# Performance work log

Hardware: AMD Instinct MI355X
Metric: run time of the kernel (lower is better)

Reference implementation:

```python
import jax, jax.numpy as jnp
import numpy as np
from jax import lax

# --- model constants (match init_kwargs) ---
B = 4096
T, N_FEAT = 100, 81
KH = 7                 # cnn_kernel_height
T_MOD = T - KH + 1     # 94
M = 100                # cnn_hidden_size
P = 128                # decoder hidden size
SKIP = 10
SH = 32                # skip_hidden_size
PT = T_MOD // SKIP     # 9


def setup_inputs() -> dict:
    key = jax.random.key(0)
    ks = jax.random.split(key, 18)
    s = 0.05
    def rn(k, shape, scale=s):
        return jax.random.normal(k, shape, dtype=jnp.float32) * scale
    return {
        "enc_data": jax.random.normal(ks[0], (B, T, N_FEAT), dtype=jnp.float32),
        # Conv2d(1 -> M, kernel=(KH, N_FEAT))
        "conv_w": rn(ks[1], (M, 1, KH, N_FEAT)),
        "conv_b": rn(ks[2], (M,)),
        # TemporalAttention: W_d: Linear(2P->M, no bias), U_d: Linear(M->M, no bias), v_d: Linear(M->1, no bias)
        "Wd": rn(ks[3], (M, 2 * P)),
        "Ud": rn(ks[4], (M, M)),
        "vd": rn(ks[5], (1, M)),
        # LSTM(input=M, hidden=P), PyTorch gate order i,f,g,o
        "lstm_wih": rn(ks[6], (4 * P, M)),
        "lstm_whh": rn(ks[7], (4 * P, P)),
        "lstm_bih": rn(ks[8], (4 * P,)),
        "lstm_bhh": rn(ks[9], (4 * P,)),
        # GRU(input=M, hidden=SH), PyTorch gate order r,z,n
        "gru_wih": rn(ks[10], (3 * SH, M)),
        "gru_whh": rn(ks[11], (3 * SH, SH)),
        "gru_bih": rn(ks[12], (3 * SH,)),
        "gru_bhh": rn(ks[13], (3 * SH,)),
        # output head: Linear(M+P+SKIP*SH -> P), ReLU, (Dropout=eval identity), Linear(P -> 1)
        "out1_w": rn(ks[14], (P, M + P + SKIP * SH)),
        "out1_b": rn(ks[15], (P,)),
        "out2_w": rn(ks[16], (1, P)),
        "out2_b": rn(ks[17], (1,)),
    }


def reference(enc_data, conv_w, conv_b, Wd, Ud, vd,
              lstm_wih, lstm_whh, lstm_bih, lstm_bhh,
              gru_wih, gru_whh, gru_bih, gru_bhh,
              out1_w, out1_b, out2_w, out2_b):
    b = enc_data.shape[0]

    # --- CNN encoder: Conv2d valid over full feature width -> [B, T_MOD, M] ---
    x = enc_data[:, None]  # [B,1,T,n]
    h = lax.conv_general_dilated(x, conv_w, window_strides=(1, 1), padding='VALID',
                                 dimension_numbers=('NCHW', 'OIHW', 'NCHW'))  # [B,M,T_MOD,1]
    H = jax.nn.relu(h + conv_b[None, :, None, None])[..., 0].transpose(0, 2, 1)  # [B,T_MOD,M]

    # precompute U_d(H) once (same math; U_d applied to H is step-invariant)
    HU = jnp.einsum('btm,km->btk', H, Ud)  # [B,T_MOD,M]

    def dec_step(carry, _):
        d, s = carry  # each [B,P]
        q = jnp.concatenate([d, s], axis=1)                       # [B,2P]
        e = jnp.tanh((q @ Wd.T)[:, None, :] + HU)                 # [B,T_MOD,M]
        scores = jnp.einsum('btm,m->bt', e, vd[0])                # [B,T_MOD]
        beta = jax.nn.softmax(scores, axis=1)                     # softmax over time
        c = jnp.einsum('bt,btm->bm', beta, H)                     # context [B,M]
        gates = c @ lstm_wih.T + lstm_bih + d @ lstm_whh.T + lstm_bhh
        i_g, f_g, g_g, o_g = jnp.split(gates, 4, axis=1)
        s_new = jax.nn.sigmoid(f_g) * s + jax.nn.sigmoid(i_g) * jnp.tanh(g_g)
        d_new = jax.nn.sigmoid(o_g) * jnp.tanh(s_new)
        return (d_new, s_new), (beta, c)

    d0 = jnp.zeros((b, P), dtype=enc_data.dtype)
    s0 = jnp.zeros((b, P), dtype=enc_data.dtype)
    (d_T, _), (betas, cs) = lax.scan(dec_step, (d0, s0), None, length=T_MOD)
    c_last = cs[-1]                                               # [B,M]
    dec_out = jnp.concatenate([d_T, c_last], axis=1)              # [B, P+M]

    # --- skip GRU over strided conv features ---
    Hs = H[:, -PT * SKIP:, :]                                     # [B, PT*SKIP, M]
    Hs = (Hs.transpose(0, 2, 1)                                   # [B, M, PT*SKIP]
            .reshape(b, M, PT, SKIP)
            .transpose(2, 0, 3, 1)                                # [PT, B, SKIP, M]
            .reshape(PT, b * SKIP, M))

    def gru_step(hprev, xt):
        gi = xt @ gru_wih.T + gru_bih
        gh = hprev @ gru_whh.T + gru_bhh
        ir, iz, inn = jnp.split(gi, 3, axis=1)
        hr, hz, hn = jnp.split(gh, 3, axis=1)
        r = jax.nn.sigmoid(ir + hr)
        z = jax.nn.sigmoid(iz + hz)
        nn_ = jnp.tanh(inn + r * hn)
        hnew = (1.0 - z) * nn_ + z * hprev
        return hnew, None

    h0 = jnp.zeros((b * SKIP, SH), dtype=enc_data.dtype)
    h_skip, _ = lax.scan(gru_step, h0, Hs)                        # [B*SKIP, SH]
    h_skip = h_skip.reshape(b, SKIP * SH)                         # matches torch view

    feat = jnp.concatenate([dec_out, h_skip], axis=1)             # [B, P+M+SKIP*SH]
    out = jax.nn.relu(feat @ out1_w.T + out1_b) @ out2_w.T + out2_b  # [B,1]
    return out[:, 0]
```

## Files before the change

### kernel.cpp

```cpp
#include <hip/hip_runtime.h>

typedef unsigned int u32;
typedef unsigned short u16;
typedef _Float16 half2_t __attribute__((ext_vector_type(2)));

#define TM 94
#define NB 4
#define DEC_NT 512

__device__ __forceinline__ float bf2f(u16 v){ return __builtin_bit_cast(float, ((u32)v)<<16); }
__device__ __forceinline__ float bflo(u32 v){ return __builtin_bit_cast(float, v<<16); }
__device__ __forceinline__ float bfhi(u32 v){ return __builtin_bit_cast(float, v & 0xffff0000u); }
__device__ __forceinline__ u32 f2bf_bits(float f){ u32 u=__builtin_bit_cast(u32,f); return (u + 0x7fffu + ((u>>16)&1u))>>16; }
__device__ __forceinline__ u32 packbf2(float a, float b){ return f2bf_bits(a) | (f2bf_bits(b)<<16); }
__device__ __forceinline__ u32 packh2(float a, float b){ half2_t h; h.x=(_Float16)a; h.y=(_Float16)b; return __builtin_bit_cast(u32,h); }
__device__ __forceinline__ float fdot2(u32 a, u32 b, float c){
  return __builtin_amdgcn_fdot2(__builtin_bit_cast(half2_t,a), __builtin_bit_cast(half2_t,b), c, false);
}
__device__ __forceinline__ float fast_rcp(float x){ return __builtin_amdgcn_rcpf(x); }
__device__ __forceinline__ float sigmoid_f(float x){ return fast_rcp(1.f + __expf(-x)); }
__device__ __forceinline__ float tanh_f(float x){ float e=__expf(2.f*x); return 1.f - 2.f*fast_rcp(e+1.f); }

__global__ __launch_bounds__(128)
void conv_kernel(const float* __restrict__ enc, const float* __restrict__ cw,
                 const float* __restrict__ cb, u16* __restrict__ Hb)
{
  __shared__ float sE[8100];
  const int tid = threadIdx.x;
  const int b = blockIdx.y;
  const int chunk = blockIdx.x;
  const float* ep = enc + (size_t)b*8100;
  for (int i=tid;i<8100;i+=128) sE[i]=ep[i];
  __syncthreads();
  if (tid >= TM) return;
  const int t = tid;
  const int mo = chunk*10;
  const float* wb = cw + mo*567;
  float acc[10];
  #pragma unroll
  for (int k=0;k<10;k++) acc[k]=cb[mo+k];
  const float* e = sE + t*81;
  #pragma unroll 3
  for (int j=0;j<567;j++){
    float ev = e[j];
    #pragma unroll
    for (int k=0;k<10;k++) acc[k] += ev*wb[k*567+j];
  }
  u32* out = (u32*)Hb + ((size_t)b*9400 + t*100 + mo)/2;
  #pragma unroll
  for (int k=0;k<5;k++) out[k] = packbf2(fmaxf(acc[2*k],0.f), fmaxf(acc[2*k+1],0.f));
}

#define OFF_SHU   75200
#define OFF_SQ2   152448
#define OFF_SA    154496
#define OFF_SB    156096
#define OFF_SC2   157632
#define OFF_SG    158464
#define OFF_SVD   162560
#define DEC_LDS   162960

__global__ __launch_bounds__(DEC_NT)
__attribute__((amdgpu_waves_per_eu(2, 2)))
void decoder_kernel(const u16* __restrict__ Hb, const float* __restrict__ Wd,
                    const float* __restrict__ Ud, const float* __restrict__ vd,
                    const float* __restrict__ wih, const float* __restrict__ whh,
                    const float* __restrict__ bih, const float* __restrict__ bhh,
                    float* __restrict__ dT, float* __restrict__ cLast)
{
  extern __shared__ char smem[];
  u16*      sH   = (u16*)smem;
  u16*      sHU  = (u16*)(smem + OFF_SHU);
  _Float16* sq2  = (_Float16*)(smem + OFF_SQ2);
  float*    sa   = (float*)(smem + OFF_SA);
  float*    sbeta= (float*)(smem + OFF_SB);
  u32*      sc2  = (u32*)(smem + OFF_SC2);
  _Float16* sg   = (_Float16*)(smem + OFF_SG);
  float*    svd  = (float*)(smem + OFF_SVD);

  const int tid = threadIdx.x;
  const int b0 = blockIdx.x * NB;

  {
    const uint4* src = (const uint4*)(Hb + (size_t)b0*9400);
    uint4* dst = (uint4*)sH;
    for (int i=tid;i<4700;i+=DEC_NT) dst[i]=src[i];
  }
  if (tid < 100) svd[tid] = vd[tid];
  {
    u32* q2 = (u32*)sq2;
    for (int i=tid;i<NB*128;i+=DEC_NT) q2[i]=0u;
  }
  __syncthreads();

  for (int idx=tid; idx<9400; idx+=DEC_NT){
    int kq = idx/376;
    int r  = idx - kq*376;
    int bi = r/94;
    int t  = r - 94*bi;
    const u32* hrow = (const u32*)sH + bi*4700 + t*50;
    const float* ud0 = Ud + (kq*4+0)*100;
    const float* ud1 = Ud + (kq*4+1)*100;
    const float* ud2 = Ud + (kq*4+2)*100;
    const float* ud3 = Ud + (kq*4+3)*100;
    float c0=0.f,c1=0.f,c2=0.f,c3=0.f;
    #pragma unroll 5
    for (int mq=0; mq<25; mq++){
      uint2 hp = *(const uint2*)(hrow + mq*2);
      float h0=bflo(hp.x), h1=bfhi(hp.x), h2=bflo(hp.y), h3=bfhi(hp.y);
      float4 u0 = *(const float4*)(ud0 + mq*4);
      float4 u1 = *(const float4*)(ud1 + mq*4);
      float4 u2 = *(const float4*)(ud2 + mq*4);
      float4 u3 = *(const float4*)(ud3 + mq*4);
      c0 += h0*u0.x + h1*u0.y + h2*u0.z + h3*u0.w;
      c1 += h0*u1.x + h1*u1.y + h2*u1.z + h3*u1.w;
      c2 += h0*u2.x + h1*u2.y + h2*u2.z + h3*u2.w;
      c3 += h0*u3.x + h1*u3.y + h2*u3.z + h3*u3.w;
    }
    u32* dst = (u32*)sHU + bi*4700 + t*50 + kq*2;
    dst[0] = packbf2(c0,c1);
    dst[1] = packbf2(c2,c3);
  }
  __syncthreads();

  __builtin_amdgcn_sched_barrier(0);
  const int mw = tid>>2, part = tid&3;
  u32 Wih[50]; u32 Whh[64]; u32 Wdf[32];
  float biasg;
  {
    const float2* wr = (const float2*)(wih + (size_t)tid*100);
    #pragma unroll
    for (int i=0;i<50;i++){ float2 v = wr[i]; Wih[i]=packh2(v.x,v.y); }
    const float2* hr = (const float2*)(whh + (size_t)tid*128);
    #pragma unroll
    for (int i=0;i<64;i++){ float2 v = hr[i]; Whh[i]=packh2(v.x,v.y); }
    biasg = bih[tid] + bhh[tid];
  }
  if (mw < 100){
    const float2* dr = (const float2*)(Wd + mw*256 + part*64);
    #pragma unroll
    for (int s=0;s<8;s++){
      int ii = (s+part)&7;
      #pragma unroll
      for (int k=0;k<4;k++){ float2 v = dr[ii*4+k]; Wdf[4*s+k]=packh2(v.x,v.y); }
    }
  }

  float s_reg = 0.f;

  for (int step=0; step<TM; step++){
    if (mw < 100){
      #pragma unroll
      for (int bi=0;bi<NB;bi++){
        const u32* qb = (const u32*)sq2 + bi*128 + part*32;
        float a0=0.f, a1=0.f;
        #pragma unroll
        for (int s=0;s<8;s++){
          int ii = (s+part)&7;
          uint4 qv = *(const uint4*)(qb + ii*4);
          a0 = fdot2(Wdf[4*s+0], qv.x, a0);
          a1 = fdot2(Wdf[4*s+1], qv.y, a1);
          a0 = fdot2(Wdf[4*s+2], qv.z, a0);
          a1 = fdot2(Wdf[4*s+3], qv.w, a1);
        }
        float acc = a0+a1;
        acc += __shfl_xor(acc,1);
        acc += __shfl_xor(acc,2);
        if (part==0) sa[bi*100+mw]=acc;
      }
    }
    __syncthreads();
    if (tid < 376){
      int bi = tid/94;
      int t  = tid - 94*bi;
      const u32* hu = (const u32*)sHU + bi*4700 + t*50;
      const float4* ap4 = (const float4*)(sa + bi*100);
      const float4* vp4 = (const float4*)svd;
      float acc=0.f;
      #pragma unroll
      for (int c=0;c<12;c++){
        uint4 h4 = ((const uint4*)hu)[c];
        float4 a0 = ap4[2*c], a1 = ap4[2*c+1];
        float4 v0 = vp4[2*c], v1 = vp4[2*c+1];
        acc += v0.x*tanh_f(a0.x + bflo(h4.x));
        acc += v0.y*tanh_f(a0.y + bfhi(h4.x));
        acc += v0.z*tanh_f(a0.z + bflo(h4.y));
        acc += v0.w*tanh_f(a0.w + bfhi(h4.y));
        acc += v1.x*tanh_f(a1.x + bflo(h4.z));
        acc += v1.y*tanh_f(a1.y + bfhi(h4.z));
        acc += v1.z*tanh_f(a1.z + bflo(h4.w));
        acc += v1.w*tanh_f(a1.w + bfhi(h4.w));
      }
      {
        uint2 ht = *(const uint2*)(hu + 48);
        float4 a = ap4[24]; float4 v = vp4[24];
        acc += v.x*tanh_f(a.x + bflo(ht.x));
        acc += v.y*tanh_f(a.y + bfhi(ht.x));
        acc += v.z*tanh_f(a.z + bflo(ht.y));
        acc += v.w*tanh_f(a.w + bfhi(ht.y));
      }
      sbeta[bi*96+t]=acc;
    }
    __syncthreads();
    if (tid < 64*NB){
      int bi = tid>>6, lane = tid&63;
      float s0 = sbeta[bi*96+lane];
      float s1 = (lane<30)? sbeta[bi*96+64+lane] : -1e30f;
      float mx = fmaxf(s0,s1);
      #pragma unroll
      for (int o=32;o>=1;o>>=1) mx = fmaxf(mx, __shfl_xor(mx,o));
      float e0 = __expf(s0-mx);
      float e1 = (lane<30)? __expf(s1-mx) : 0.f;
      float sm = e0+e1;
      #pragma unroll
      for (int o=32;o>=1;o>>=1) sm += __shfl_xor(sm,o);
      float rs = fast_rcp(sm);
      sbeta[bi*96+lane] = e0*rs;
      if (lane<30) sbeta[bi*96+64+lane] = e1*rs;
    }
    __syncthreads();
    if (tid < 400){
      int bi = tid/100;
      int r  = tid - 100*bi;
      int mp = r>>1, th = r&1;
      const float* bp = sbeta + bi*96 + th*47;
      const u32* hp = (const u32*)sH + bi*4700 + th*47*50 + mp;
      float a0=0.f, a1=0.f;
      #pragma unroll
      for (int i=0;i<47;i++){
        float be = bp[i];
        u32 h = hp[i*50];
        a0 += be*bflo(h); a1 += be*bfhi(h);
      }
      a0 += __shfl_xor(a0,1);
      a1 += __shfl_xor(a1,1);
      if (th==0){
        sc2[bi*52+mp] = packh2(a0,a1);
        if (step==TM-1){
          cLast[(size_t)(b0+bi)*100 + 2*mp]   = a0;
          cLast[(size_t)(b0+bi)*100 + 2*mp+1] = a1;
        }
      }
    }
    __syncthreads();
    #pragma unroll
    for (int bi=0;bi<NB;bi++){
      float a0 = biasg, a1 = 0.f;
      const uint4* cp = (const uint4*)(sc2 + bi*52);
      #pragma unroll
      for (int i=0;i<12;i++){
        uint4 cv = cp[i];
        a0 = fdot2(Wih[4*i+0], cv.x, a0);
        a1 = fdot2(Wih[4*i+1], cv.y, a1);
        a0 = fdot2(Wih[4*i+2], cv.z, a0);
        a1 = fdot2(Wih[4*i+3], cv.w, a1);
      }
      {
        const u32* ct = sc2 + bi*52 + 48;
        a0 = fdot2(Wih[48], ct[0], a0);
        a1 = fdot2(Wih[49], ct[1], a1);
      }
      const uint4* qp = (const uint4*)((const u32*)sq2 + bi*128);
      #pragma unroll
      for (int i=0;i<16;i++){
        uint4 qv = qp[i];
        a0 = fdot2(Whh[4*i+0], qv.x, a0);
        a1 = fdot2(Whh[4*i+1], qv.y, a1);
        a0 = fdot2(Whh[4*i+2], qv.z, a0);
        a1 = fdot2(Whh[4*i+3], qv.w, a1);
      }
      sg[bi*512+tid] = (_Float16)(a0+a1);
    }
    __syncthreads();
    {
      int bi = tid>>7, p = tid&127;
      float ig = (float)sg[bi*512+p];
      float fg = (float)sg[bi*512+128+p];
      float gg = (float)sg[bi*512+256+p];
      float og = (float)sg[bi*512+384+p];
      float sn = sigmoid_f(fg)*s_reg + sigmoid_f(ig)*tanh_f(gg);
      float dn = sigmoid_f(og)*tanh_f(sn);
      s_reg = sn;
      sq2[bi*256+p]=(_Float16)dn;
      sq2[bi*256+128+p]=(_Float16)sn;
      if (step==TM-1) dT[(size_t)(b0+bi)*128+p]=dn;
    }
    __syncthreads();
  }
}

__global__ __launch_bounds__(256)
void gru_kernel(const u16* __restrict__ Hb, const float* __restrict__ wih,
                const float* __restrict__ whh, const float* __restrict__ bihp,
                const float* __restrict__ bhhp, float* __restrict__ hskip)
{
  __shared__ float sWih[96][101];
  __shared__ float sWhh[96][33];
  __shared__ float sxt[8][100];
  __shared__ float sh[8][33];
  const int tid = threadIdx.x;
  for (int i=tid;i<9600;i+=256){ sWih[i/100][i%100]=wih[i]; }
  for (int i=tid;i<3072;i+=256){ sWhh[i>>5][i&31]=whh[i]; }
  const int r = tid>>5, j = tid&31;
  const int rowg = blockIdx.x*8 + r;
  const int b = rowg/10, sk = rowg - b*10;
  const float b_r = bihp[j], b_z = bihp[32+j], b_n = bihp[64+j];
  const float hb_r = bhhp[j], hb_z = bhhp[32+j], hb_n = bhhp[64+j];
  sh[r][j]=0.f;
  float h = 0.f;
  __syncthreads();
  for (int pt=0; pt<9; pt++){
    for (int i=tid;i<800;i+=256){
      int rr=i/100, m=i-rr*100;
      int rg = blockIdx.x*8+rr; int bb=rg/10, ss=rg-bb*10;
      sxt[rr][m] = bf2f(Hb[(size_t)bb*9400 + (size_t)(4+pt*10+ss)*100 + m]);
    }
    __syncthreads();
    float gi_r=b_r, gi_z=b_z, gi_n=b_n, gh_r=hb_r, gh_z=hb_z, gh_n=hb_n;
    #pragma unroll 4
    for (int m=0;m<100;m++){
      float x = sxt[r][m];
      gi_r += sWih[j][m]*x; gi_z += sWih[32+j][m]*x; gi_n += sWih[64+j][m]*x;
    }
    #pragma unroll
    for (int k=0;k<32;k++){
      float hp = sh[r][k];
      gh_r += sWhh[j][k]*hp; gh_z += sWhh[32+j][k]*hp; gh_n += sWhh[64+j][k]*hp;
    }
    float rg_ = sigmoid_f(gi_r+gh_r);
    float z  = sigmoid_f(gi_z+gh_z);
    float n  = tanh_f(gi_n + rg_*gh_n);
    h = (1.f-z)*n + z*h;
    __syncthreads();
    sh[r][j]=h;
    __syncthreads();
  }
  hskip[(size_t)b*320 + sk*32 + j] = h;
}

#define OUT_NB 32
#define OUT_LDS ((OUT_NB*552 + 8*552)*4)

__global__ __launch_bounds__(256)
void out_kernel(const float* __restrict__ dT, const float* __restrict__ cLast,
                const float* __restrict__ hskip, const float* __restrict__ w1,
                const float* __restrict__ b1, const float* __restrict__ w2,
                const float* __restrict__ b2, float* __restrict__ outp)
{
  extern __shared__ float osm[];
  float* sf = osm;
  float* sw = osm + OUT_NB*552;
  const int tid = threadIdx.x;
  const int b0 = blockIdx.x*OUT_NB;
  for (int i=tid;i<OUT_NB*548;i+=256){
    int bl = i/548, k = i - 548*bl; int b = b0+bl;
    float v;
    if (k<128) v = dT[(size_t)b*128+k];
    else if (k<228) v = cLast[(size_t)b*100+(k-128)];
    else v = hskip[(size_t)b*320+(k-228)];
    sf[bl*552+k]=v;
  }
  const int bl = tid>>3, j = tid&7;
  float outv = 0.f;
  for (int jt=0; jt<128; jt+=8){
    __syncthreads();
    for (int i=tid;i<8*548;i+=256){
      int rr=i/548, c=i-548*rr;
      sw[rr*552+c] = w1[(size_t)jt*548 + i];
    }
    __syncthreads();
    float acc = b1[jt+j];
    const float* fr = sf + bl*552;
    const float* wr = sw + j*552;
    #pragma unroll 4
    for (int k=0;k<548;k++) acc += fr[k]*wr[k];
    outv += fmaxf(acc,0.f)*w2[jt+j];
  }
  outv += __shfl_xor(outv,1);
  outv += __shfl_xor(outv,2);
  outv += __shfl_xor(outv,4);
  if (j==0) outp[b0+bl] = outv + b2[0];
}

extern "C" void kernel_launch(void* const* d_in, const int* in_sizes, int n_in,
                              void* d_out, int out_size, void* d_ws, size_t ws_size,
                              hipStream_t stream)
{
  const float* enc      = (const float*)d_in[0];
  const float* conv_w   = (const float*)d_in[1];
  const float* conv_b   = (const float*)d_in[2];
  const float* Wd       = (const float*)d_in[3];
  const float* Ud       = (const float*)d_in[4];
  const float* vd       = (const float*)d_in[5];
  const float* lstm_wih = (const float*)d_in[6];
  const float* lstm_whh = (const float*)d_in[7];
  const float* lstm_bih = (const float*)d_in[8];
  const float* lstm_bhh = (const float*)d_in[9];
  const float* gru_wih  = (const float*)d_in[10];
  const float* gru_whh  = (const float*)d_in[11];
  const float* gru_bih  = (const float*)d_in[12];
  const float* gru_bhh  = (const float*)d_in[13];
  const float* out1_w   = (const float*)d_in[14];
  const float* out1_b   = (const float*)d_in[15];
  const float* out2_w   = (const float*)d_in[16];
  const float* out2_b   = (const float*)d_in[17];

  char* ws = (char*)d_ws;
  u16*   Hb    = (u16*)ws;
  float* dT    = (float*)(ws + 77004800);
  float* cLast = (float*)(ws + 79101952);
  float* hskip = (float*)(ws + 80740352);

  conv_kernel<<<dim3(10,4096,1), 128, 0, stream>>>(enc, conv_w, conv_b, Hb);

  (void)hipFuncSetAttribute((const void*)decoder_kernel,
                            hipFuncAttributeMaxDynamicSharedMemorySize, DEC_LDS);
  decoder_kernel<<<4096/NB, DEC_NT, DEC_LDS, stream>>>(Hb, Wd, Ud, vd,
                                                       lstm_wih, lstm_whh, lstm_bih, lstm_bhh,
                                                       dT, cLast);

  gru_kernel<<<5120, 256, 0, stream>>>(Hb, gru_wih, gru_whh, gru_bih, gru_bhh, hskip);

  (void)hipFuncSetAttribute((const void*)out_kernel,
                            hipFuncAttributeMaxDynamicSharedMemorySize, OUT_LDS);
  out_kernel<<<4096/OUT_NB, 256, OUT_LDS, stream>>>(dT, cLast, hskip, out1_w, out1_b,
                                                    out2_w, out2_b, (float*)d_out);
}
```

Before: 8.340 ms.

## Double decoder block to 1024 threads and split per-step work across halves

Raises the decoder block from 512 to 1024 threads and splits each stage of the per-step recurrence more finely. The attention projection, score, and context stages get more threads per output, combined with extra shuffles. The LSTM gate matvec is split into two halves, one doing Wih plus part of Whh and the other the rest of Whh, with partial sums in two LDS buffers that are added later. This shortens the serial per-step critical path and reduces weights held in registers per thread. The cost is more shuffles and syncs across 16 waves, and fp16 partial gate sums add rounding.

```diff
diff --git a/kernel.cpp b/kernel.cpp
--- a/kernel.cpp
+++ b/kernel.cpp
@@ -6,7 +6,7 @@
 
 #define TM 94
 #define NB 4
-#define DEC_NT 512
+#define DEC_NT 1024
 
 __device__ __forceinline__ float bf2f(u16 v){ return __builtin_bit_cast(float, ((u32)v)<<16); }
 __device__ __forceinline__ float bflo(u32 v){ return __builtin_bit_cast(float, v<<16); }
@@ -51,17 +51,15 @@
   for (int k=0;k<5;k++) out[k] = packbf2(fmaxf(acc[2*k],0.f), fmaxf(acc[2*k+1],0.f));
 }
 
-#define OFF_SHU   75200
-#define OFF_SQ2   152448
-#define OFF_SA    154496
-#define OFF_SB    156096
-#define OFF_SC2   157632
-#define OFF_SG    158464
-#define OFF_SVD   162560
-#define DEC_LDS   162960
-
-__global__ __launch_bounds__(DEC_NT)
-__attribute__((amdgpu_waves_per_eu(2, 2)))
+#define OFF_SHU 75200
+#define OFF_SQ2 150400
+#define OFF_SC2 152448
+#define OFF_SVD 153280
+#define OFF_AB  153680
+#define DEC_LDS 161872
+
+__global__ __launch_bounds__(DEC_NT, 4)
+__attribute__((amdgpu_waves_per_eu(4, 4)))
 void decoder_kernel(const u16* __restrict__ Hb, const float* __restrict__ Wd,
                     const float* __restrict__ Ud, const float* __restrict__ vd,
                     const float* __restrict__ wih, const float* __restrict__ whh,
@@ -72,11 +70,12 @@
   u16*      sH   = (u16*)smem;
   u16*      sHU  = (u16*)(smem + OFF_SHU);
   _Float16* sq2  = (_Float16*)(smem + OFF_SQ2);
-  float*    sa   = (float*)(smem + OFF_SA);
-  float*    sbeta= (float*)(smem + OFF_SB);
   u32*      sc2  = (u32*)(smem + OFF_SC2);
-  _Float16* sg   = (_Float16*)(smem + OFF_SG);
   float*    svd  = (float*)(smem + OFF_SVD);
+  float*    sa   = (float*)(smem + OFF_AB);
+  float*    sbeta= (float*)(smem + OFF_AB + 1600);
+  _Float16* sgA  = (_Float16*)(smem + OFF_AB);
+  _Float16* sgB  = (_Float16*)(smem + OFF_AB + 4096);
 
   const int tid = threadIdx.x;
   const int b0 = blockIdx.x * NB;
@@ -122,27 +121,36 @@
     dst[1] = packbf2(c2,c3);
   }
   __syncthreads();
-
   __builtin_amdgcn_sched_barrier(0);
-  const int mw = tid>>2, part = tid&3;
-  u32 Wih[50]; u32 Whh[64]; u32 Wdf[32];
-  float biasg;
-  {
-    const float2* wr = (const float2*)(wih + (size_t)tid*100);
-    #pragma unroll
-    for (int i=0;i<50;i++){ float2 v = wr[i]; Wih[i]=packh2(v.x,v.y); }
-    const float2* hr = (const float2*)(whh + (size_t)tid*128);
-    #pragma unroll
-    for (int i=0;i<64;i++){ float2 v = hr[i]; Whh[i]=packh2(v.x,v.y); }
-    biasg = bih[tid] + bhh[tid];
-  }
+
+  const int half = tid >> 9;
+  const int g    = tid & 511;
+  u32 WA[58];
+  float biasg = 0.f;
+  if (half == 0){
+    const float2* wr = (const float2*)(wih + (size_t)g*100);
+    #pragma unroll
+    for (int i=0;i<50;i++){ float2 v = wr[i]; WA[i]=packh2(v.x,v.y); }
+    const float2* hr = (const float2*)(whh + (size_t)g*128);
+    #pragma unroll
+    for (int i=0;i<8;i++){ float2 v = hr[i]; WA[50+i]=packh2(v.x,v.y); }
+    biasg = bih[g] + bhh[g];
+  } else {
+    const float2* hr = (const float2*)(whh + (size_t)g*128 + 16);
+    #pragma unroll
+    for (int i=0;i<56;i++){ float2 v = hr[i]; WA[i]=packh2(v.x,v.y); }
+  }
+  const int mw = tid>>3, part = tid&7;
+  u32 Wdf[16];
   if (mw < 100){
-    const float2* dr = (const float2*)(Wd + mw*256 + part*64);
-    #pragma unroll
-    for (int s=0;s<8;s++){
-      int ii = (s+part)&7;
+    const float* wd = Wd + mw*256 + part*32;
+    #pragma unroll
+    for (int i=0;i<4;i++){
+      int ii = (i+part)&3;
       #pragma unroll
-      for (int k=0;k<4;k++){ float2 v = dr[ii*4+k]; Wdf[4*s+k]=packh2(v.x,v.y); }
+      for (int k=0;k<4;k++){
+        Wdf[4*i+k] = packh2(wd[ii*8+2*k], wd[ii*8+2*k+1]);
+      }
     }
   }
 
@@ -150,38 +158,40 @@
 
   for (int step=0; step<TM; step++){
     if (mw < 100){
-      #pragma unroll
+      #pragma unroll 1
       for (int bi=0;bi<NB;bi++){
-        const u32* qb = (const u32*)sq2 + bi*128 + part*32;
+        const u32* qb = (const u32*)sq2 + bi*128 + part*16;
         float a0=0.f, a1=0.f;
         #pragma unroll
-        for (int s=0;s<8;s++){
-          int ii = (s+part)&7;
+        for (int i=0;i<4;i++){
+          int ii = (i+part)&3;
           uint4 qv = *(const uint4*)(qb + ii*4);
-          a0 = fdot2(Wdf[4*s+0], qv.x, a0);
-          a1 = fdot2(Wdf[4*s+1], qv.y, a1);
-          a0 = fdot2(Wdf[4*s+2], qv.z, a0);
-          a1 = fdot2(Wdf[4*s+3], qv.w, a1);
+          a0 = fdot2(Wdf[4*i+0], qv.x, a0);
+          a1 = fdot2(Wdf[4*i+1], qv.y, a1);
+          a0 = fdot2(Wdf[4*i+2], qv.z, a0);
+          a1 = fdot2(Wdf[4*i+3], qv.w, a1);
         }
         float acc = a0+a1;
         acc += __shfl_xor(acc,1);
         acc += __shfl_xor(acc,2);
+        acc += __shfl_xor(acc,4);
         if (part==0) sa[bi*100+mw]=acc;
       }
     }
     __syncthreads();
-    if (tid < 376){
-      int bi = tid/94;
-      int t  = tid - 94*bi;
-      const u32* hu = (const u32*)sHU + bi*4700 + t*50;
-      const float4* ap4 = (const float4*)(sa + bi*100);
-      const float4* vp4 = (const float4*)svd;
+    if (tid < 752){
+      int row = tid>>1, th = tid&1;
+      int bi = row/94;
+      int t  = row - 94*bi;
+      const uint4* hu4 = (const uint4*)((const u32*)sHU + bi*4700 + t*50 + th*24);
+      const float4* ap = (const float4*)(sa + bi*100) + th*12;
+      const float4* vp = (const float4*)svd + th*12;
       float acc=0.f;
       #pragma unroll
-      for (int c=0;c<12;c++){
-        uint4 h4 = ((const uint4*)hu)[c];
-        float4 a0 = ap4[2*c], a1 = ap4[2*c+1];
-        float4 v0 = vp4[2*c], v1 = vp4[2*c+1];
+      for (int c=0;c<6;c++){
+        uint4 h4 = hu4[c];
+        float4 a0 = ap[2*c], a1 = ap[2*c+1];
+        float4 v0 = vp[2*c], v1 = vp[2*c+1];
         acc += v0.x*tanh_f(a0.x + bflo(h4.x));
         acc += v0.y*tanh_f(a0.y + bfhi(h4.x));
         acc += v0.z*tanh_f(a0.z + bflo(h4.y));
@@ -191,15 +201,16 @@
         acc += v1.z*tanh_f(a1.z + bflo(h4.w));
         acc += v1.w*tanh_f(a1.w + bfhi(h4.w));
       }
-      {
-        uint2 ht = *(const uint2*)(hu + 48);
-        float4 a = ap4[24]; float4 v = vp4[24];
+      if (th){
+        uint2 ht = *(const uint2*)((const u32*)hu4 + 24);
+        float4 a = ap[12]; float4 v = vp[12];
         acc += v.x*tanh_f(a.x + bflo(ht.x));
         acc += v.y*tanh_f(a.y + bfhi(ht.x));
         acc += v.z*tanh_f(a.z + bflo(ht.y));
         acc += v.w*tanh_f(a.w + bfhi(ht.y));
       }
-      sbeta[bi*96+t]=acc;
+      acc += __shfl_xor(acc,1);
+      if (!th) sbeta[bi*96+t]=acc;
     }
     __syncthreads();
     if (tid < 64*NB){
@@ -219,21 +230,26 @@
       if (lane<30) sbeta[bi*96+64+lane] = e1*rs;
     }
     __syncthreads();
-    if (tid < 400){
-      int bi = tid/100;
-      int r  = tid - 100*bi;
-      int mp = r>>1, th = r&1;
-      const float* bp = sbeta + bi*96 + th*47;
-      const u32* hp = (const u32*)sH + bi*4700 + th*47*50 + mp;
+    if (tid < 800){
+      int bi = tid/200;
+      int r  = tid - 200*bi;
+      int mp = r>>2, th = r&3;
+      int tstart = (th<2) ? th*24 : 48+(th-2)*23;
+      const float* bp = sbeta + bi*96 + tstart;
+      const u32* hp = (const u32*)sH + bi*4700 + tstart*50 + mp;
       float a0=0.f, a1=0.f;
       #pragma unroll
-      for (int i=0;i<47;i++){
+      for (int i=0;i<23;i++){
         float be = bp[i];
         u32 h = hp[i*50];
         a0 += be*bflo(h); a1 += be*bfhi(h);
       }
-      a0 += __shfl_xor(a0,1);
-      a1 += __shfl_xor(a1,1);
+      if (th<2){
+        float be = bp[23]; u32 h = hp[23*50];
+        a0 += be*bflo(h); a1 += be*bfhi(h);
+      }
+      a0 += __shfl_xor(a0,1); a1 += __shfl_xor(a1,1);
+      a0 += __shfl_xor(a0,2); a1 += __shfl_xor(a1,2);
       if (th==0){
         sc2[bi*52+mp] = packh2(a0,a1);
         if (step==TM-1){
@@ -243,41 +259,58 @@
       }
     }
     __syncthreads();
-    #pragma unroll
-    for (int bi=0;bi<NB;bi++){
-      float a0 = biasg, a1 = 0.f;
-      const uint4* cp = (const uint4*)(sc2 + bi*52);
-      #pragma unroll
-      for (int i=0;i<12;i++){
-        uint4 cv = cp[i];
-        a0 = fdot2(Wih[4*i+0], cv.x, a0);
-        a1 = fdot2(Wih[4*i+1], cv.y, a1);
-        a0 = fdot2(Wih[4*i+2], cv.z, a0);
-        a1 = fdot2(Wih[4*i+3], cv.w, a1);
-      }
-      {
-        const u32* ct = sc2 + bi*52 + 48;
-        a0 = fdot2(Wih[48], ct[0], a0);
-        a1 = fdot2(Wih[49], ct[1], a1);
-      }
-      const uint4* qp = (const uint4*)((const u32*)sq2 + bi*128);
-      #pragma unroll
-      for (int i=0;i<16;i++){
-        uint4 qv = qp[i];
-        a0 = fdot2(Whh[4*i+0], qv.x, a0);
-        a1 = fdot2(Whh[4*i+1], qv.y, a1);
-        a0 = fdot2(Whh[4*i+2], qv.z, a0);
-        a1 = fdot2(Whh[4*i+3], qv.w, a1);
-      }
-      sg[bi*512+tid] = (_Float16)(a0+a1);
-    }
-    __syncthreads();
-    {
+    if (half == 0){
+      #pragma unroll 1
+      for (int bi=0;bi<NB;bi++){
+        float a0 = biasg, a1 = 0.f;
+        const uint4* cp = (const uint4*)(sc2 + bi*52);
+        #pragma unroll
+        for (int i=0;i<12;i++){
+          uint4 cv = cp[i];
+          a0 = fdot2(WA[4*i+0], cv.x, a0);
+          a1 = fdot2(WA[4*i+1], cv.y, a1);
+          a0 = fdot2(WA[4*i+2], cv.z, a0);
+          a1 = fdot2(WA[4*i+3], cv.w, a1);
+        }
+        {
+          const u32* ct = sc2 + bi*52 + 48;
+          a0 = fdot2(WA[48], ct[0], a0);
+          a1 = fdot2(WA[49], ct[1], a1);
+        }
+        const uint4* qp = (const uint4*)((const u32*)sq2 + bi*128);
+        #pragma unroll
+        for (int i=0;i<2;i++){
+          uint4 qv = qp[i];
+          a0 = fdot2(WA[50+4*i+0], qv.x, a0);
+          a1 = fdot2(WA[50+4*i+1], qv.y, a1);
+          a0 = fdot2(WA[50+4*i+2], qv.z, a0);
+          a1 = fdot2(WA[50+4*i+3], qv.w, a1);
+        }
+        sgA[bi*512+g] = (_Float16)(a0+a1);
+      }
+    } else {
+      #pragma unroll 1
+      for (int bi=0;bi<NB;bi++){
+        float a0 = 0.f, a1 = 0.f;
+        const uint4* qp = (const uint4*)((const u32*)sq2 + bi*128);
+        #pragma unroll
+        for (int i=0;i<14;i++){
+          uint4 qv = qp[2+i];
+          a0 = fdot2(WA[4*i+0], qv.x, a0);
+          a1 = fdot2(WA[4*i+1], qv.y, a1);
+          a0 = fdot2(WA[4*i+2], qv.z, a0);
+          a1 = fdot2(WA[4*i+3], qv.w, a1);
+        }
+        sgB[bi*512+g] = (_Float16)(a0+a1);
+      }
+    }
+    __syncthreads();
+    if (tid < 512){
       int bi = tid>>7, p = tid&127;
-      float ig = (float)sg[bi*512+p];
-      float fg = (float)sg[bi*512+128+p];
-      float gg = (float)sg[bi*512+256+p];
-      float og = (float)sg[bi*512+384+p];
+      float ig = (float)sgA[bi*512+p]       + (float)sgB[bi*512+p];
+      float fg = (float)sgA[bi*512+128+p]   + (float)sgB[bi*512+128+p];
+      float gg = (float)sgA[bi*512+256+p]   + (float)sgB[bi*512+256+p];
+      float og = (float)sgA[bi*512+384+p]   + (float)sgB[bi*512+384+p];
       float sn = sigmoid_f(fg)*s_reg + sigmoid_f(ig)*tanh_f(gg);
       float dn = sigmoid_f(og)*tanh_f(sn);
       s_reg = sn;
```

New measurement: 7.632 ms. 1.09x faster.
